# Optimization experiments

Hardware: AMD Instinct MI355X
Metric: run time of the kernel (lower is better)

## Reference

```python
import jax, jax.numpy as jnp
import numpy as np

# sparse_shape = output_shape[1:4] + [1,0,0], num_input_frames=1 -> grid [41,128,128]
B, D, H, W = 1, 41, 128, 128
CIN = 16
N = 40000  # active voxels
DN = ('NDHWC', 'DHWIO', 'NDHWC')
# 11 convs of the SparseSequential, in order
KSHAPES = [(3,3,3,CIN,32), (3,3,3,32,32), (3,3,3,32,64)] + [(3,3,3,64,64)]*7 + [(3,1,1,64,64)]
P1 = ((1,1),(1,1),(1,1))   # padding [1,1,1]
P2 = ((0,0),(1,1),(1,1))   # padding [0,1,1]
P0 = ((0,0),(0,0),(0,0))   # no padding


def conv3d(x, w, stride, pad):
    return jax.lax.conv_general_dilated(x, w, stride, pad, dimension_numbers=DN)


def occupancy(mask, ksz, stride, pad):
    # active output sites of a strided SparseConv3d = any active input in receptive field
    ones = jnp.ones(ksz + (1, 1), jnp.float32)
    return conv3d(mask[..., None].astype(jnp.float32), ones, stride, pad)[..., 0] > 0


def forward(feats, coords, ws, ss, bs):
    idx = (coords[:, 0], coords[:, 1], coords[:, 2], coords[:, 3])
    grid = jnp.zeros((B, D, H, W, CIN), feats.dtype).at[idx].set(feats)
    mask0 = jnp.zeros((B, D, H, W), bool).at[idx].set(True)

    def bnrelu(x, i, m):
        # eval-mode BatchNorm1d folded to per-channel scale/bias, applied only on active voxels
        return jnp.maximum(x * ss[i] + bs[i], 0.0) * m[..., None]

    # SubMConv3d layers keep the active set of their input (mask applied after BN+ReLU)
    x = bnrelu(conv3d(grid, ws[0], (1, 1, 1), P1), 0, mask0)
    x = bnrelu(conv3d(x, ws[1], (1, 1, 1), P1), 1, mask0)
    # SpConv3d 32->64, stride (2,1,1), pad [1,1,1]
    mask1 = occupancy(mask0, (3, 3, 3), (2, 1, 1), P1)
    x = bnrelu(conv3d(x, ws[2], (2, 1, 1), P1), 2, mask1)
    for i in (3, 4, 5):
        x = bnrelu(conv3d(x, ws[i], (1, 1, 1), P1), i, mask1)
    # SpConv3d 64->64, stride (2,1,1), pad [0,1,1]
    mask2 = occupancy(mask1, (3, 3, 3), (2, 1, 1), P2)
    x = bnrelu(conv3d(x, ws[6], (2, 1, 1), P2), 6, mask2)
    for i in (7, 8, 9):
        x = bnrelu(conv3d(x, ws[i], (1, 1, 1), P1), i, mask2)
    # SpConv3d 64->64, kernel (3,1,1), stride (2,1,1), no pad
    mask3 = occupancy(mask2, (3, 1, 1), (2, 1, 1), P0)
    x = bnrelu(conv3d(x, ws[10], (2, 1, 1), P0), 10, mask3)
    return x  # [1, 4, 128, 128, 64]


def setup_inputs():
    key = jax.random.key(0)
    ks = jax.random.split(key, 4 + 3 * 11)
    feats = jax.random.normal(ks[0], (N, CIN), jnp.float32)
    z = jax.random.randint(ks[1], (N,), 0, D)
    y = jax.random.randint(ks[2], (N,), 0, H)
    x = jax.random.randint(ks[3], (N,), 0, W)
    coords = jnp.stack([jnp.zeros((N,), jnp.int32), z, y, x], axis=1)
    inp = {"voxel_features": feats, "coords": coords}
    for i, shp in enumerate(KSHAPES):
        fan = shp[0] * shp[1] * shp[2] * shp[3]
        inp[f"w{i}"] = jax.random.normal(ks[4 + 3 * i], shp, jnp.float32) / np.sqrt(fan).astype(np.float32)
        inp[f"s{i}"] = 1.0 + 0.1 * jax.random.normal(ks[5 + 3 * i], (shp[4],), jnp.float32)
        inp[f"b{i}"] = 0.1 * jax.random.normal(ks[6 + 3 * i], (shp[4],), jnp.float32)
    return inp


def reference(voxel_features, coords, w0, w1, w2, w3, w4, w5, w6, w7, w8, w9, w10,
              s0, s1, s2, s3, s4, s5, s6, s7, s8, s9, s10,
              b0, b1, b2, b3, b4, b5, b6, b7, b8, b9, b10):
    ws = [w0, w1, w2, w3, w4, w5, w6, w7, w8, w9, w10]
    ss = [s0, s1, s2, s3, s4, s5, s6, s7, s8, s9, s10]
    bs = [b0, b1, b2, b3, b4, b5, b6, b7, b8, b9, b10]
    return forward(voxel_features, coords, ws, ss, bs)
```

## Files before the change

### kernel.cpp

```cpp
#include <hip/hip_runtime.h>
#include <hip/hip_bf16.h>
#include <stdint.h>


typedef _Float16 h8 __attribute__((ext_vector_type(8)));
typedef float f4 __attribute__((ext_vector_type(4)));

#define HCONST 128
#define WCONST 128

__global__ void scatter_owner_kernel(const int* __restrict__ coords,
                                     int* __restrict__ owner,
                                     unsigned char* __restrict__ mask0, int N) {
    int n = blockIdx.x * blockDim.x + threadIdx.x;
    if (n >= N) return;
    int z = coords[n * 4 + 1];
    int y = coords[n * 4 + 2];
    int x = coords[n * 4 + 3];
    int pos = (z * HCONST + y) * WCONST + x;
    atomicMax(&owner[pos], n);
    mask0[pos] = 1;
}

__global__ void scatter_write_kernel(const float* __restrict__ feats,
                                     const int* __restrict__ coords,
                                     const int* __restrict__ owner,
                                     _Float16* __restrict__ grid, int N) {
    int n = blockIdx.x * blockDim.x + threadIdx.x;
    if (n >= N) return;
    int z = coords[n * 4 + 1];
    int y = coords[n * 4 + 2];
    int x = coords[n * 4 + 3];
    int pos = (z * HCONST + y) * WCONST + x;
    if (owner[pos] != n) return;
    _Float16* d = grid + (size_t)pos * 32;
#pragma unroll
    for (int c = 0; c < 16; ++c) d[c] = (_Float16)feats[(size_t)n * 16 + c];
}

template <int KD, int KHW, int SD, int PD, int PHW>
__global__ void occupancy_kernel(const unsigned char* __restrict__ min_,
                                 unsigned char* __restrict__ mout,
                                 int Din, int Dout) {
    int idx = blockIdx.x * blockDim.x + threadIdx.x;
    int total = Dout * HCONST * WCONST;
    if (idx >= total) return;
    int ow = idx % WCONST;
    int oh = (idx / WCONST) % HCONST;
    int od = idx / (WCONST * HCONST);
    unsigned char r = 0;
    for (int kd = 0; kd < KD; ++kd) {
        int d = od * SD - PD + kd;
        if (d < 0 || d >= Din) continue;
        for (int kh = 0; kh < KHW; ++kh) {
            int h = oh - PHW + kh;
            if ((unsigned)h >= (unsigned)HCONST) continue;
            for (int kw = 0; kw < KHW; ++kw) {
                int w = ow - PHW + kw;
                if ((unsigned)w >= (unsigned)WCONST) continue;
                r |= min_[(d * HCONST + h) * WCONST + w];
            }
        }
    }
    mout[idx] = r ? 1 : 0;
}

__global__ void prep_w_kernel(const float* __restrict__ src, _Float16* __restrict__ dst,
                              int K3, int CIN, int CINP, int COUT) {
    int idx = blockIdx.x * blockDim.x + threadIdx.x;
    int total = K3 * CINP * COUT;
    if (idx >= total) return;
    int j  = idx & 7;
    int t  = idx >> 3;
    int co = t % COUT; t /= COUT;
    int lq = t & 3;    t >>= 2;
    int KSP = CINP / 32;
    int ks = t % KSP;
    int k  = t / KSP;
    int ci = ks * 32 + lq * 8 + j;
    float v = (ci < CIN) ? src[((size_t)k * CIN + ci) * COUT + co] : 0.f;
    dst[idx] = (_Float16)v;
}

template <int CIN, int COUT, int KD, int KHW, int SD, int PD, int PHW, bool OUT_F32>
__global__ __launch_bounds__(256) void conv_mfma_kernel(
    const _Float16* __restrict__ X, const _Float16* __restrict__ Wt,
    const float* __restrict__ scale, const float* __restrict__ bias,
    const unsigned char* __restrict__ mask, void* __restrict__ outv,
    int Din) {
    constexpr int KW = KHW, KH = KHW;
    constexpr int KS = CIN / 32;
    constexpr int NWAVE = COUT / 2;
    constexpr int NFRAG = NWAVE / 16;
    constexpr int PWOFF = (KHW == 3) ? 1 : 0;
    constexpr int WINW = 64 + 2 * PWOFF;
    constexpr int CINB = CIN * 2;
    constexpr int CPR = CIN / 8;
    constexpr int CHUNKS = KH * WINW * CPR;
    constexpr int NIT = (CHUNKS + 255) / 256;

    __shared__ char lds[KH * WINW * CINB];

    const int tid = threadIdx.x;
    const int lane = tid & 63, wave = tid >> 6;
    const int wm = wave & 1, wn = wave >> 1;
    const int lm = lane & 15, lq = lane >> 4;
    const int wbase = blockIdx.x * 64;
    const int oh = blockIdx.y, od = blockIdx.z;

    f4 acc[2][NFRAG];
#pragma unroll
    for (int mt = 0; mt < 2; ++mt)
#pragma unroll
        for (int nf = 0; nf < NFRAG; ++nf) acc[mt][nf] = (f4){0.f, 0.f, 0.f, 0.f};

    for (int kd = 0; kd < KD; ++kd) {
        int din = od * SD - PD + kd;
        if (din < 0 || din >= Din) continue;
        __syncthreads();
        const _Float16* sbase = X + (size_t)din * 128 * 128 * CIN;
#pragma unroll
        for (int it = 0; it < NIT; ++it) {
            int c = tid + it * 256;
            if (c < CHUNKS) {
                int r  = c / CPR;
                int cq = c % CPR;
                int khr = r / WINW;
                int lw  = r % WINW;
                int hin = oh - PHW + khr;
                int w   = wbase + lw - PWOFF;
                uint4 v = {0u, 0u, 0u, 0u};
                if ((unsigned)hin < 128u && (unsigned)w < 128u)
                    v = *(const uint4*)(sbase + ((size_t)hin * 128 + w) * CIN + cq * 8);
                int byte = r * CINB + ((cq * 16) ^ ((r & (CPR - 1)) << 4));
                *(uint4*)(lds + byte) = v;
            }
        }
        __syncthreads();
#pragma unroll
        for (int kh = 0; kh < KH; ++kh) {
            h8 Bf[KW][KS][NFRAG];
            const _Float16* wbaseW = Wt + (size_t)(kd * KH + kh) * KW * KS * 4 * COUT * 8;
#pragma unroll
            for (int kw = 0; kw < KW; ++kw)
#pragma unroll
                for (int ks = 0; ks < KS; ++ks)
#pragma unroll
                    for (int nf = 0; nf < NFRAG; ++nf) {
                        int co = wn * NWAVE + nf * 16 + lm;
                        Bf[kw][ks][nf] =
                            *(const h8*)(wbaseW + (((size_t)(kw * KS + ks) * 4 + lq) * COUT + co) * 8);
                    }
#pragma unroll
            for (int kw = 0; kw < KW; ++kw)
#pragma unroll
                for (int ks = 0; ks < KS; ++ks) {
                    h8 Af[2];
#pragma unroll
                    for (int mt = 0; mt < 2; ++mt) {
                        int lw = wm * 32 + mt * 16 + lm + kw;
                        int r = kh * WINW + lw;
                        int byte = r * CINB + ((ks * 64 + lq * 16) ^ ((r & (CPR - 1)) << 4));
                        Af[mt] = *(const h8*)(lds + byte);
                    }
#pragma unroll
                    for (int mt = 0; mt < 2; ++mt)
#pragma unroll
                        for (int nf = 0; nf < NFRAG; ++nf)
                            acc[mt][nf] = __builtin_amdgcn_mfma_f32_16x16x32_f16(
                                Af[mt], Bf[kw][ks][nf], acc[mt][nf], 0, 0, 0);
                }
        }
    }

    const unsigned char* mrow = mask + ((size_t)od * 128 + oh) * 128 + wbase;
    size_t obase = (((size_t)od * 128 + oh) * 128 + wbase) * COUT;
#pragma unroll
    for (int nf = 0; nf < NFRAG; ++nf) {
        int co = wn * NWAVE + nf * 16 + lm;
        float s = scale[co];
        float b = bias[co];
#pragma unroll
        for (int mt = 0; mt < 2; ++mt) {
            int w0 = wm * 32 + mt * 16 + lq * 4;
#pragma unroll
            for (int r = 0; r < 4; ++r) {
                float y = fmaxf(acc[mt][nf][r] * s + b, 0.f);
                y = mrow[w0 + r] ? y : 0.f;
                if (OUT_F32)
                    ((float*)outv)[obase + (size_t)(w0 + r) * COUT + co] = y;
                else
                    ((_Float16*)outv)[obase + (size_t)(w0 + r) * COUT + co] = (_Float16)y;
            }
        }
    }
}

extern "C" void kernel_launch(void* const* d_in, const int* in_sizes, int n_in,
                              void* d_out, int out_size, void* d_ws, size_t ws_size,
                              hipStream_t stream) {
    const float* feats  = (const float*)d_in[0];
    const int*   coords = (const int*)d_in[1];
    const float* W_[11]; const float* S_[11]; const float* B_[11];
    for (int i = 0; i < 11; ++i) {
        W_[i] = (const float*)d_in[2 + 3 * i];
        S_[i] = (const float*)d_in[3 + 3 * i];
        B_[i] = (const float*)d_in[4 + 3 * i];
    }
    const int N = in_sizes[0] / 16;

    char* ws = (char*)d_ws;
    size_t off = 0;
    auto alloc = [&](size_t bytes) {
        void* p = ws + off;
        off = (off + bytes + 255) & ~(size_t)255;
        return p;
    };
    const size_t BUF_BYTES = (size_t)22020096 * 2;
    _Float16* buf0 = (_Float16*)alloc(BUF_BYTES);
    _Float16* buf1 = (_Float16*)alloc(BUF_BYTES);
    unsigned char* m0 = (unsigned char*)alloc(671744);
    unsigned char* m1 = (unsigned char*)alloc(344064);
    unsigned char* m2 = (unsigned char*)alloc(163840);
    unsigned char* m3 = (unsigned char*)alloc(65536);
    int* owner = (int*)alloc((size_t)671744 * 4);
    static const int WT_SZ[11] = {27*32*32, 27*32*32, 27*64*32,
                                  27*64*64, 27*64*64, 27*64*64, 27*64*64,
                                  27*64*64, 27*64*64, 27*64*64, 3*64*64};
    _Float16* Wt[11];
    for (int i = 0; i < 11; ++i) Wt[i] = (_Float16*)alloc((size_t)WT_SZ[i] * 2);
    (void)ws_size; (void)n_in; (void)out_size;

    _Float16* grid0 = buf1;
    const size_t GRID_BYTES = (size_t)671744 * 32 * 2;

    hipMemsetAsync(grid0, 0, GRID_BYTES, stream);
    hipMemsetAsync(m0, 0, 671744, stream);
    hipMemsetAsync(owner, 0xFF, (size_t)671744 * 4, stream);

    scatter_owner_kernel<<<(N + 255) / 256, 256, 0, stream>>>(coords, owner, m0, N);
    scatter_write_kernel<<<(N + 255) / 256, 256, 0, stream>>>(feats, coords, owner, grid0, N);

    occupancy_kernel<3, 3, 2, 1, 1><<<(21 * 128 * 128 + 255) / 256, 256, 0, stream>>>(m0, m1, 41, 21);
    occupancy_kernel<3, 3, 2, 0, 1><<<(10 * 128 * 128 + 255) / 256, 256, 0, stream>>>(m1, m2, 21, 10);
    occupancy_kernel<3, 1, 2, 0, 0><<<(4 * 128 * 128 + 255) / 256, 256, 0, stream>>>(m2, m3, 10, 4);

    {
        static const int K3[11]   = {27,27,27,27,27,27,27,27,27,27,3};
        static const int CI[11]   = {16,32,32,64,64,64,64,64,64,64,64};
        static const int CIP[11]  = {32,32,32,64,64,64,64,64,64,64,64};
        static const int CO[11]   = {32,32,64,64,64,64,64,64,64,64,64};
        for (int i = 0; i < 11; ++i) {
            int total = K3[i] * CO[i] * CIP[i];
            prep_w_kernel<<<(total + 255) / 256, 256, 0, stream>>>(W_[i], Wt[i], K3[i], CI[i], CIP[i], CO[i]);
        }
    }

    conv_mfma_kernel<32, 32, 3, 3, 1, 1, 1, false><<<dim3(2, 128, 41), 256, 0, stream>>>(
        grid0, Wt[0], S_[0], B_[0], m0, buf0, 41);
    conv_mfma_kernel<32, 32, 3, 3, 1, 1, 1, false><<<dim3(2, 128, 41), 256, 0, stream>>>(
        buf0, Wt[1], S_[1], B_[1], m0, buf1, 41);
    conv_mfma_kernel<32, 64, 3, 3, 2, 1, 1, false><<<dim3(2, 128, 21), 256, 0, stream>>>(
        buf1, Wt[2], S_[2], B_[2], m1, buf0, 41);
    conv_mfma_kernel<64, 64, 3, 3, 1, 1, 1, false><<<dim3(2, 128, 21), 256, 0, stream>>>(
        buf0, Wt[3], S_[3], B_[3], m1, buf1, 21);
    conv_mfma_kernel<64, 64, 3, 3, 1, 1, 1, false><<<dim3(2, 128, 21), 256, 0, stream>>>(
        buf1, Wt[4], S_[4], B_[4], m1, buf0, 21);
    conv_mfma_kernel<64, 64, 3, 3, 1, 1, 1, false><<<dim3(2, 128, 21), 256, 0, stream>>>(
        buf0, Wt[5], S_[5], B_[5], m1, buf1, 21);
    conv_mfma_kernel<64, 64, 3, 3, 2, 0, 1, false><<<dim3(2, 128, 10), 256, 0, stream>>>(
        buf1, Wt[6], S_[6], B_[6], m2, buf0, 21);
    conv_mfma_kernel<64, 64, 3, 3, 1, 1, 1, false><<<dim3(2, 128, 10), 256, 0, stream>>>(
        buf0, Wt[7], S_[7], B_[7], m2, buf1, 10);
    conv_mfma_kernel<64, 64, 3, 3, 1, 1, 1, false><<<dim3(2, 128, 10), 256, 0, stream>>>(
        buf1, Wt[8], S_[8], B_[8], m2, buf0, 10);
    conv_mfma_kernel<64, 64, 3, 3, 1, 1, 1, false><<<dim3(2, 128, 10), 256, 0, stream>>>(
        buf0, Wt[9], S_[9], B_[9], m2, buf1, 10);
    conv_mfma_kernel<64, 64, 3, 1, 2, 0, 0, true><<<dim3(2, 128, 4), 256, 0, stream>>>(
        buf1, Wt[10], S_[10], B_[10], m3, (float*)d_out, 10);
}
```

Measured before the change: 930.4 us.

## Switch conv to 32x32x16 MFMA with full-row tiles and per-kh LDS staging

The conv kernel now uses 32x32x16 f16 MFMA instructions instead of 16x16x32. Each block covers a full 128-wide output row with 2 waves, each wave computing all output channels. The input is staged one input row at a time per kh, with a barrier pair per kh, in place of all three rows at once. The weight prep layout is changed to match the new K-split. Fewer, larger blocks and more barriers could lower occupancy and reduce overlap of loads with compute.

```diff
diff --git a/kernel.cpp b/kernel.cpp
--- a/kernel.cpp
+++ b/kernel.cpp
@@ -4,7 +4,7 @@
 
 
 typedef _Float16 h8 __attribute__((ext_vector_type(8)));
-typedef float f4 __attribute__((ext_vector_type(4)));
+typedef float f16v __attribute__((ext_vector_type(16)));
 
 #define HCONST 128
 #define WCONST 128
@@ -73,124 +73,122 @@
     int j  = idx & 7;
     int t  = idx >> 3;
     int co = t % COUT; t /= COUT;
-    int lq = t & 3;    t >>= 2;
-    int KSP = CINP / 32;
+    int half = t & 1;  t >>= 1;
+    int KSP = CINP / 16;
     int ks = t % KSP;
     int k  = t / KSP;
-    int ci = ks * 32 + lq * 8 + j;
+    int ci = ks * 16 + half * 8 + j;
     float v = (ci < CIN) ? src[((size_t)k * CIN + ci) * COUT + co] : 0.f;
     dst[idx] = (_Float16)v;
 }
 
 template <int CIN, int COUT, int KD, int KHW, int SD, int PD, int PHW, bool OUT_F32>
-__global__ __launch_bounds__(256) void conv_mfma_kernel(
+__global__ __launch_bounds__(128) void conv_mfma_kernel(
     const _Float16* __restrict__ X, const _Float16* __restrict__ Wt,
     const float* __restrict__ scale, const float* __restrict__ bias,
     const unsigned char* __restrict__ mask, void* __restrict__ outv,
     int Din) {
     constexpr int KW = KHW, KH = KHW;
-    constexpr int KS = CIN / 32;
-    constexpr int NWAVE = COUT / 2;
-    constexpr int NFRAG = NWAVE / 16;
+    constexpr int KS = CIN / 16;
+    constexpr int NFRAG = COUT / 32;
     constexpr int PWOFF = (KHW == 3) ? 1 : 0;
-    constexpr int WINW = 64 + 2 * PWOFF;
+    constexpr int WIN = 128 + 2 * PWOFF;
     constexpr int CINB = CIN * 2;
     constexpr int CPR = CIN / 8;
-    constexpr int CHUNKS = KH * WINW * CPR;
-    constexpr int NIT = (CHUNKS + 255) / 256;
-
-    __shared__ char lds[KH * WINW * CINB];
+    constexpr int CHUNKS = WIN * CPR;
+    constexpr int NIT = (CHUNKS + 127) / 128;
+
+    __shared__ char lds[WIN * CINB];
 
     const int tid = threadIdx.x;
-    const int lane = tid & 63, wave = tid >> 6;
-    const int wm = wave & 1, wn = wave >> 1;
-    const int lm = lane & 15, lq = lane >> 4;
-    const int wbase = blockIdx.x * 64;
-    const int oh = blockIdx.y, od = blockIdx.z;
-
-    f4 acc[2][NFRAG];
+    const int lane = tid & 63, wm = tid >> 6;
+    const int lr = lane & 31, lh = lane >> 5;
+    const int oh = blockIdx.x, od = blockIdx.y;
+
+    f16v acc[2][NFRAG];
 #pragma unroll
     for (int mt = 0; mt < 2; ++mt)
 #pragma unroll
-        for (int nf = 0; nf < NFRAG; ++nf) acc[mt][nf] = (f4){0.f, 0.f, 0.f, 0.f};
+        for (int nf = 0; nf < NFRAG; ++nf)
+#pragma unroll
+            for (int e = 0; e < 16; ++e) acc[mt][nf][e] = 0.f;
 
     for (int kd = 0; kd < KD; ++kd) {
         int din = od * SD - PD + kd;
         if (din < 0 || din >= Din) continue;
-        __syncthreads();
-        const _Float16* sbase = X + (size_t)din * 128 * 128 * CIN;
-#pragma unroll
-        for (int it = 0; it < NIT; ++it) {
-            int c = tid + it * 256;
-            if (c < CHUNKS) {
-                int r  = c / CPR;
-                int cq = c % CPR;
-                int khr = r / WINW;
-                int lw  = r % WINW;
-                int hin = oh - PHW + khr;
-                int w   = wbase + lw - PWOFF;
-                uint4 v = {0u, 0u, 0u, 0u};
-                if ((unsigned)hin < 128u && (unsigned)w < 128u)
-                    v = *(const uint4*)(sbase + ((size_t)hin * 128 + w) * CIN + cq * 8);
-                int byte = r * CINB + ((cq * 16) ^ ((r & (CPR - 1)) << 4));
-                *(uint4*)(lds + byte) = v;
-            }
-        }
-        __syncthreads();
 #pragma unroll
         for (int kh = 0; kh < KH; ++kh) {
-            h8 Bf[KW][KS][NFRAG];
-            const _Float16* wbaseW = Wt + (size_t)(kd * KH + kh) * KW * KS * 4 * COUT * 8;
-#pragma unroll
-            for (int kw = 0; kw < KW; ++kw)
+            int hin = oh - PHW + kh;
+            if ((unsigned)hin >= 128u) continue;
+            __syncthreads();
+            const _Float16* src = X + (((size_t)din * 128 + hin) * 128) * CIN;
+#pragma unroll
+            for (int it = 0; it < NIT; ++it) {
+                int c = tid + it * 128;
+                if (c < CHUNKS) {
+                    int r  = c / CPR;
+                    int cq = c % CPR;
+                    int w  = r - PWOFF;
+                    uint4 v = {0u, 0u, 0u, 0u};
+                    if ((unsigned)w < 128u)
+                        v = *(const uint4*)(src + (size_t)w * CIN + cq * 8);
+                    int byte = r * CINB + ((cq * 16) ^ ((r & (CPR - 1)) << 4));
+                    *(uint4*)(lds + byte) = v;
+                }
+            }
+            __syncthreads();
+            const _Float16* wb = Wt + (size_t)(kd * KH + kh) * KW * KS * 2 * COUT * 8;
+#pragma unroll
+            for (int kw = 0; kw < KW; ++kw) {
+                h8 Bf[KS][NFRAG];
 #pragma unroll
                 for (int ks = 0; ks < KS; ++ks)
 #pragma unroll
                     for (int nf = 0; nf < NFRAG; ++nf) {
-                        int co = wn * NWAVE + nf * 16 + lm;
-                        Bf[kw][ks][nf] =
-                            *(const h8*)(wbaseW + (((size_t)(kw * KS + ks) * 4 + lq) * COUT + co) * 8);
+                        int co = nf * 32 + lr;
+                        Bf[ks][nf] = *(const h8*)(
+                            wb + (((size_t)(kw * KS + ks) * 2 + lh) * COUT + co) * 8);
                     }
-#pragma unroll
-            for (int kw = 0; kw < KW; ++kw)
 #pragma unroll
                 for (int ks = 0; ks < KS; ++ks) {
                     h8 Af[2];
 #pragma unroll
                     for (int mt = 0; mt < 2; ++mt) {
-                        int lw = wm * 32 + mt * 16 + lm + kw;
-                        int r = kh * WINW + lw;
-                        int byte = r * CINB + ((ks * 64 + lq * 16) ^ ((r & (CPR - 1)) << 4));
+                        int row = wm * 64 + mt * 32 + lr + kw;
+                        int byte = row * CINB +
+                                   ((ks * 32 + lh * 16) ^ ((row & (CPR - 1)) << 4));
                         Af[mt] = *(const h8*)(lds + byte);
                     }
 #pragma unroll
                     for (int mt = 0; mt < 2; ++mt)
 #pragma unroll
                         for (int nf = 0; nf < NFRAG; ++nf)
-                            acc[mt][nf] = __builtin_amdgcn_mfma_f32_16x16x32_f16(
-                                Af[mt], Bf[kw][ks][nf], acc[mt][nf], 0, 0, 0);
+                            acc[mt][nf] = __builtin_amdgcn_mfma_f32_32x32x16_f16(
+                                Af[mt], Bf[ks][nf], acc[mt][nf], 0, 0, 0);
                 }
-        }
-    }
-
-    const unsigned char* mrow = mask + ((size_t)od * 128 + oh) * 128 + wbase;
-    size_t obase = (((size_t)od * 128 + oh) * 128 + wbase) * COUT;
+            }
+        }
+    }
+
+    const unsigned char* mrow = mask + ((size_t)od * 128 + oh) * 128;
+    size_t obase = (((size_t)od * 128 + oh) * 128) * COUT;
 #pragma unroll
     for (int nf = 0; nf < NFRAG; ++nf) {
-        int co = wn * NWAVE + nf * 16 + lm;
+        int co = nf * 32 + lr;
         float s = scale[co];
         float b = bias[co];
 #pragma unroll
         for (int mt = 0; mt < 2; ++mt) {
-            int w0 = wm * 32 + mt * 16 + lq * 4;
-#pragma unroll
-            for (int r = 0; r < 4; ++r) {
+#pragma unroll
+            for (int r = 0; r < 16; ++r) {
+                int wrow = (r & 3) + 8 * (r >> 2) + 4 * lh;
+                int w = wm * 64 + mt * 32 + wrow;
                 float y = fmaxf(acc[mt][nf][r] * s + b, 0.f);
-                y = mrow[w0 + r] ? y : 0.f;
+                y = mrow[w] ? y : 0.f;
                 if (OUT_F32)
-                    ((float*)outv)[obase + (size_t)(w0 + r) * COUT + co] = y;
+                    ((float*)outv)[obase + (size_t)w * COUT + co] = y;
                 else
-                    ((_Float16*)outv)[obase + (size_t)(w0 + r) * COUT + co] = (_Float16)y;
+                    ((_Float16*)outv)[obase + (size_t)w * COUT + co] = (_Float16)y;
             }
         }
     }
@@ -256,26 +254,26 @@
         }
     }
 
-    conv_mfma_kernel<32, 32, 3, 3, 1, 1, 1, false><<<dim3(2, 128, 41), 256, 0, stream>>>(
+    conv_mfma_kernel<32, 32, 3, 3, 1, 1, 1, false><<<dim3(128, 41), 128, 0, stream>>>(
         grid0, Wt[0], S_[0], B_[0], m0, buf0, 41);
-    conv_mfma_kernel<32, 32, 3, 3, 1, 1, 1, false><<<dim3(2, 128, 41), 256, 0, stream>>>(
+    conv_mfma_kernel<32, 32, 3, 3, 1, 1, 1, false><<<dim3(128, 41), 128, 0, stream>>>(
         buf0, Wt[1], S_[1], B_[1], m0, buf1, 41);
-    conv_mfma_kernel<32, 64, 3, 3, 2, 1, 1, false><<<dim3(2, 128, 21), 256, 0, stream>>>(
+    conv_mfma_kernel<32, 64, 3, 3, 2, 1, 1, false><<<dim3(128, 21), 128, 0, stream>>>(
         buf1, Wt[2], S_[2], B_[2], m1, buf0, 41);
-    conv_mfma_kernel<64, 64, 3, 3, 1, 1, 1, false><<<dim3(2, 128, 21), 256, 0, stream>>>(
+    conv_mfma_kernel<64, 64, 3, 3, 1, 1, 1, false><<<dim3(128, 21), 128, 0, stream>>>(
         buf0, Wt[3], S_[3], B_[3], m1, buf1, 21);
-    conv_mfma_kernel<64, 64, 3, 3, 1, 1, 1, false><<<dim3(2, 128, 21), 256, 0, stream>>>(
+    conv_mfma_kernel<64, 64, 3, 3, 1, 1, 1, false><<<dim3(128, 21), 128, 0, stream>>>(
         buf1, Wt[4], S_[4], B_[4], m1, buf0, 21);
-    conv_mfma_kernel<64, 64, 3, 3, 1, 1, 1, false><<<dim3(2, 128, 21), 256, 0, stream>>>(
+    conv_mfma_kernel<64, 64, 3, 3, 1, 1, 1, false><<<dim3(128, 21), 128, 0, stream>>>(
         buf0, Wt[5], S_[5], B_[5], m1, buf1, 21);
-    conv_mfma_kernel<64, 64, 3, 3, 2, 0, 1, false><<<dim3(2, 128, 10), 256, 0, stream>>>(
+    conv_mfma_kernel<64, 64, 3, 3, 2, 0, 1, false><<<dim3(128, 10), 128, 0, stream>>>(
         buf1, Wt[6], S_[6], B_[6], m2, buf0, 21);
-    conv_mfma_kernel<64, 64, 3, 3, 1, 1, 1, false><<<dim3(2, 128, 10), 256, 0, stream>>>(
+    conv_mfma_kernel<64, 64, 3, 3, 1, 1, 1, false><<<dim3(128, 10), 128, 0, stream>>>(
         buf0, Wt[7], S_[7], B_[7], m2, buf1, 10);
-    conv_mfma_kernel<64, 64, 3, 3, 1, 1, 1, false><<<dim3(2, 128, 10), 256, 0, stream>>>(
+    conv_mfma_kernel<64, 64, 3, 3, 1, 1, 1, false><<<dim3(128, 10), 128, 0, stream>>>(
         buf1, Wt[8], S_[8], B_[8], m2, buf0, 10);
-    conv_mfma_kernel<64, 64, 3, 3, 1, 1, 1, false><<<dim3(2, 128, 10), 256, 0, stream>>>(
+    conv_mfma_kernel<64, 64, 3, 3, 1, 1, 1, false><<<dim3(128, 10), 128, 0, stream>>>(
         buf0, Wt[9], S_[9], B_[9], m2, buf1, 10);
-    conv_mfma_kernel<64, 64, 3, 1, 2, 0, 0, true><<<dim3(2, 128, 4), 256, 0, stream>>>(
+    conv_mfma_kernel<64, 64, 3, 1, 2, 0, 0, true><<<dim3(128, 4), 128, 0, stream>>>(
         buf1, Wt[10], S_[10], B_[10], m3, (float*)d_out, 10);
 }
```

Result: slower. 1.264 ms (+35.8%).

## Give each wave all output channels and remap blocks XCD-aware

Applied to the files above, without the earlier changes.

Changes the wave work split so each of the four waves owns 16 output positions across all COUT channels, instead of a 2x2 split over positions and channels. Each wave now loads the full set of weight fragments per kw, and each A fragment is reused across all NFRAG MFMAs. It also switches to a 1D grid with a block-index swizzle that groups consecutive tiles onto the same XCD, aiming for better L2 locality of shared input rows. The trade-offs are more global weight loads per wave and different register pressure. The swizzle assumes the grid size is divisible by 8.

```diff
diff --git a/kernel.cpp b/kernel.cpp
--- a/kernel.cpp
+++ b/kernel.cpp
@@ -90,8 +90,7 @@
     int Din) {
     constexpr int KW = KHW, KH = KHW;
     constexpr int KS = CIN / 32;
-    constexpr int NWAVE = COUT / 2;
-    constexpr int NFRAG = NWAVE / 16;
+    constexpr int NFRAG = COUT / 16;
     constexpr int PWOFF = (KHW == 3) ? 1 : 0;
     constexpr int WINW = 64 + 2 * PWOFF;
     constexpr int CINB = CIN * 2;
@@ -103,16 +102,17 @@
 
     const int tid = threadIdx.x;
     const int lane = tid & 63, wave = tid >> 6;
-    const int wm = wave & 1, wn = wave >> 1;
     const int lm = lane & 15, lq = lane >> 4;
-    const int wbase = blockIdx.x * 64;
-    const int oh = blockIdx.y, od = blockIdx.z;
-
-    f4 acc[2][NFRAG];
-#pragma unroll
-    for (int mt = 0; mt < 2; ++mt)
-#pragma unroll
-        for (int nf = 0; nf < NFRAG; ++nf) acc[mt][nf] = (f4){0.f, 0.f, 0.f, 0.f};
+    const int cpx = gridDim.x >> 3;
+    const int bid = blockIdx.x;
+    const int d   = (bid & 7) * cpx + (bid >> 3);
+    const int wbase = (d & 1) * 64;
+    const int oh = (d >> 1) & 127;
+    const int od = d >> 8;
+
+    f4 acc[NFRAG];
+#pragma unroll
+    for (int nf = 0; nf < NFRAG; ++nf) acc[nf] = (f4){0.f, 0.f, 0.f, 0.f};
 
     for (int kd = 0; kd < KD; ++kd) {
         int din = od * SD - PD + kd;
@@ -139,37 +139,30 @@
         __syncthreads();
 #pragma unroll
         for (int kh = 0; kh < KH; ++kh) {
-            h8 Bf[KW][KS][NFRAG];
             const _Float16* wbaseW = Wt + (size_t)(kd * KH + kh) * KW * KS * 4 * COUT * 8;
 #pragma unroll
-            for (int kw = 0; kw < KW; ++kw)
+            for (int kw = 0; kw < KW; ++kw) {
+                h8 Bf[KS][NFRAG];
 #pragma unroll
                 for (int ks = 0; ks < KS; ++ks)
 #pragma unroll
                     for (int nf = 0; nf < NFRAG; ++nf) {
-                        int co = wn * NWAVE + nf * 16 + lm;
-                        Bf[kw][ks][nf] =
+                        int co = nf * 16 + lm;
+                        Bf[ks][nf] =
                             *(const h8*)(wbaseW + (((size_t)(kw * KS + ks) * 4 + lq) * COUT + co) * 8);
                     }
 #pragma unroll
-            for (int kw = 0; kw < KW; ++kw)
-#pragma unroll
                 for (int ks = 0; ks < KS; ++ks) {
-                    h8 Af[2];
-#pragma unroll
-                    for (int mt = 0; mt < 2; ++mt) {
-                        int lw = wm * 32 + mt * 16 + lm + kw;
-                        int r = kh * WINW + lw;
-                        int byte = r * CINB + ((ks * 64 + lq * 16) ^ ((r & (CPR - 1)) << 4));
-                        Af[mt] = *(const h8*)(lds + byte);
-                    }
-#pragma unroll
-                    for (int mt = 0; mt < 2; ++mt)
-#pragma unroll
-                        for (int nf = 0; nf < NFRAG; ++nf)
-                            acc[mt][nf] = __builtin_amdgcn_mfma_f32_16x16x32_f16(
-                                Af[mt], Bf[kw][ks][nf], acc[mt][nf], 0, 0, 0);
+                    int lw = wave * 16 + lm + kw;
+                    int r = kh * WINW + lw;
+                    int byte = r * CINB + ((ks * 64 + lq * 16) ^ ((r & (CPR - 1)) << 4));
+                    h8 Af = *(const h8*)(lds + byte);
+#pragma unroll
+                    for (int nf = 0; nf < NFRAG; ++nf)
+                        acc[nf] = __builtin_amdgcn_mfma_f32_16x16x32_f16(
+                            Af, Bf[ks][nf], acc[nf], 0, 0, 0);
                 }
+            }
         }
     }
 
@@ -177,21 +170,18 @@
     size_t obase = (((size_t)od * 128 + oh) * 128 + wbase) * COUT;
 #pragma unroll
     for (int nf = 0; nf < NFRAG; ++nf) {
-        int co = wn * NWAVE + nf * 16 + lm;
+        int co = nf * 16 + lm;
         float s = scale[co];
         float b = bias[co];
-#pragma unroll
-        for (int mt = 0; mt < 2; ++mt) {
-            int w0 = wm * 32 + mt * 16 + lq * 4;
-#pragma unroll
-            for (int r = 0; r < 4; ++r) {
-                float y = fmaxf(acc[mt][nf][r] * s + b, 0.f);
-                y = mrow[w0 + r] ? y : 0.f;
-                if (OUT_F32)
-                    ((float*)outv)[obase + (size_t)(w0 + r) * COUT + co] = y;
-                else
-                    ((_Float16*)outv)[obase + (size_t)(w0 + r) * COUT + co] = (_Float16)y;
-            }
+        int w0 = wave * 16 + lq * 4;
+#pragma unroll
+        for (int r = 0; r < 4; ++r) {
+            float y = fmaxf(acc[nf][r] * s + b, 0.f);
+            y = mrow[w0 + r] ? y : 0.f;
+            if (OUT_F32)
+                ((float*)outv)[obase + (size_t)(w0 + r) * COUT + co] = y;
+            else
+                ((_Float16*)outv)[obase + (size_t)(w0 + r) * COUT + co] = (_Float16)y;
         }
     }
 }
@@ -256,26 +246,26 @@
         }
     }
 
-    conv_mfma_kernel<32, 32, 3, 3, 1, 1, 1, false><<<dim3(2, 128, 41), 256, 0, stream>>>(
+    conv_mfma_kernel<32, 32, 3, 3, 1, 1, 1, false><<<2 * 128 * 41, 256, 0, stream>>>(
         grid0, Wt[0], S_[0], B_[0], m0, buf0, 41);
-    conv_mfma_kernel<32, 32, 3, 3, 1, 1, 1, false><<<dim3(2, 128, 41), 256, 0, stream>>>(
+    conv_mfma_kernel<32, 32, 3, 3, 1, 1, 1, false><<<2 * 128 * 41, 256, 0, stream>>>(
         buf0, Wt[1], S_[1], B_[1], m0, buf1, 41);
-    conv_mfma_kernel<32, 64, 3, 3, 2, 1, 1, false><<<dim3(2, 128, 21), 256, 0, stream>>>(
+    conv_mfma_kernel<32, 64, 3, 3, 2, 1, 1, false><<<2 * 128 * 21, 256, 0, stream>>>(
         buf1, Wt[2], S_[2], B_[2], m1, buf0, 41);
-    conv_mfma_kernel<64, 64, 3, 3, 1, 1, 1, false><<<dim3(2, 128, 21), 256, 0, stream>>>(
+    conv_mfma_kernel<64, 64, 3, 3, 1, 1, 1, false><<<2 * 128 * 21, 256, 0, stream>>>(
         buf0, Wt[3], S_[3], B_[3], m1, buf1, 21);
-    conv_mfma_kernel<64, 64, 3, 3, 1, 1, 1, false><<<dim3(2, 128, 21), 256, 0, stream>>>(
+    conv_mfma_kernel<64, 64, 3, 3, 1, 1, 1, false><<<2 * 128 * 21, 256, 0, stream>>>(
         buf1, Wt[4], S_[4], B_[4], m1, buf0, 21);
-    conv_mfma_kernel<64, 64, 3, 3, 1, 1, 1, false><<<dim3(2, 128, 21), 256, 0, stream>>>(
+    conv_mfma_kernel<64, 64, 3, 3, 1, 1, 1, false><<<2 * 128 * 21, 256, 0, stream>>>(
         buf0, Wt[5], S_[5], B_[5], m1, buf1, 21);
-    conv_mfma_kernel<64, 64, 3, 3, 2, 0, 1, false><<<dim3(2, 128, 10), 256, 0, stream>>>(
+    conv_mfma_kernel<64, 64, 3, 3, 2, 0, 1, false><<<2 * 128 * 10, 256, 0, stream>>>(
         buf1, Wt[6], S_[6], B_[6], m2, buf0, 21);
-    conv_mfma_kernel<64, 64, 3, 3, 1, 1, 1, false><<<dim3(2, 128, 10), 256, 0, stream>>>(
+    conv_mfma_kernel<64, 64, 3, 3, 1, 1, 1, false><<<2 * 128 * 10, 256, 0, stream>>>(
         buf0, Wt[7], S_[7], B_[7], m2, buf1, 10);
-    conv_mfma_kernel<64, 64, 3, 3, 1, 1, 1, false><<<dim3(2, 128, 10), 256, 0, stream>>>(
+    conv_mfma_kernel<64, 64, 3, 3, 1, 1, 1, false><<<2 * 128 * 10, 256, 0, stream>>>(
         buf1, Wt[8], S_[8], B_[8], m2, buf0, 10);
-    conv_mfma_kernel<64, 64, 3, 3, 1, 1, 1, false><<<dim3(2, 128, 10), 256, 0, stream>>>(
+    conv_mfma_kernel<64, 64, 3, 3, 1, 1, 1, false><<<2 * 128 * 10, 256, 0, stream>>>(
         buf0, Wt[9], S_[9], B_[9], m2, buf1, 10);
-    conv_mfma_kernel<64, 64, 3, 1, 2, 0, 0, true><<<dim3(2, 128, 4), 256, 0, stream>>>(
+    conv_mfma_kernel<64, 64, 3, 1, 2, 0, 0, true><<<2 * 128 * 4, 256, 0, stream>>>(
         buf1, Wt[10], S_[10], B_[10], m3, (float*)d_out, 10);
 }
```

New measurement: 1.409 ms. +51.4%, slower.
